# Kernel tuning notes

Hardware: AMD Instinct MI355X
Metric: run time of the kernel (lower is better)

The kernel has to match this reference:

```python
import jax, jax.numpy as jnp
import numpy as np

TEMPERATURE = 0.07


def setup_inputs() -> dict:
    key = jax.random.key(0)
    k1, k2 = jax.random.split(key)
    features = jax.random.normal(k1, (8192, 512), dtype=jnp.float32)
    targets = jax.random.randint(k2, (8192,), 0, 100, dtype=jnp.int64)
    return {"features": features, "targets": targets}


def reference(features, targets):
    n = features.shape[0]
    # L2 normalize along feature dim (F.normalize, dim=1)
    feats = features / jnp.linalg.norm(features, axis=1, keepdims=True)
    # [N, N] similarity matrix
    sim = jnp.matmul(feats, feats.T) / TEMPERATURE
    # positive-pair mask (same label, excluding self)
    mask = (targets[:, None] == targets[None, :]).astype(sim.dtype)
    mask = mask - jnp.eye(n, dtype=sim.dtype)
    # log_prob = sim - log(sum_j exp(sim_ij)) ; denominator includes the diagonal,
    # exactly as in the torch code. logsumexp is the stable single-pass form.
    log_prob = sim - jax.nn.logsumexp(sim, axis=1, keepdims=True)
    mean_log_prob_pos = jnp.sum(mask * log_prob, axis=1) / jnp.sum(mask, axis=1)
    loss = -jnp.mean(mean_log_prob_pos)
    return loss
```

## Files before the change

### kernel.cpp

```cpp
#include <hip/hip_runtime.h>

#define TEMP 0.07f
#define NSLOT 41

typedef __attribute__((ext_vector_type(4))) float f32x4;
typedef __attribute__((ext_vector_type(4))) int   i32x4;
typedef __attribute__((ext_vector_type(8))) int   i32x8;

__global__ __launch_bounds__(256) void knorm(const float* __restrict__ X,
                                             unsigned char* __restrict__ Fq, int D) {
  int row = blockIdx.x * 4 + (threadIdx.x >> 6);
  int lane = threadIdx.x & 63;
  const float4* xr = (const float4*)(X + (size_t)row * D);
  float4 a = xr[lane];
  float4 b = xr[lane + 64];
  float ss = a.x*a.x + a.y*a.y + a.z*a.z + a.w*a.w
           + b.x*b.x + b.y*b.y + b.z*b.z + b.w*b.w;
  #pragma unroll
  for (int off = 1; off < 64; off <<= 1) ss += __shfl_xor(ss, off, 64);
  float r = rsqrtf(ss);
  int lo = 0, hi = 0;
  lo = __builtin_amdgcn_cvt_pk_fp8_f32(a.x*r, a.y*r, lo, false);
  lo = __builtin_amdgcn_cvt_pk_fp8_f32(a.z*r, a.w*r, lo, true);
  hi = __builtin_amdgcn_cvt_pk_fp8_f32(b.x*r, b.y*r, hi, false);
  hi = __builtin_amdgcn_cvt_pk_fp8_f32(b.z*r, b.w*r, hi, true);
  unsigned char* op = Fq + (size_t)row * D;
  *(int*)(op + lane * 4)       = lo;
  *(int*)(op + 256 + lane * 4) = hi;
}

__global__ __launch_bounds__(256, 1)
void kmain(const unsigned char* __restrict__ F, const int* __restrict__ tgt,
           float* __restrict__ psum, float* __restrict__ pmask, int N, int D) {
  __shared__ __align__(16) unsigned char Bs[2][64 * 512];
  __shared__ float cred[2][4][128];
  __shared__ int tgts[512];

  const int tid  = threadIdx.x;
  const int lane = tid & 63;
  const int wave = tid >> 6;
  const int quad = lane >> 4;
  const int l15  = lane & 15;

  const int b = blockIdx.x;
  int I, t0, ntiles;
  if (b < 512) { I = b & 63; t0 = (b >> 6) * 4; ntiles = 4; }
  else         { I = b - 512; t0 = 32;          ntiles = 1; }
  const int rowbase = I * 128;
  int cb[4];
  #pragma unroll
  for (int c = 0; c < 4; ++c) cb[c] = ((I + t0 + c) & 63) << 7;

  i32x8 af[2][4];
  #pragma unroll
  for (int mi = 0; mi < 2; ++mi) {
    const unsigned char* rp = F + (size_t)(rowbase + wave*32 + mi*16 + l15) * 512 + quad*32;
    #pragma unroll
    for (int ks = 0; ks < 4; ++ks) {
      i32x4 lo = *(const i32x4*)(rp + ks*128);
      i32x4 hi = *(const i32x4*)(rp + ks*128 + 16);
      af[mi][ks] = __builtin_shufflevector(lo, hi, 0,1,2,3,4,5,6,7);
    }
  }

  int trow[2][4];
  #pragma unroll
  for (int mi = 0; mi < 2; ++mi)
    #pragma unroll
    for (int r = 0; r < 4; ++r)
      trow[mi][r] = tgt[rowbase + wave*32 + mi*16 + quad*4 + r];

  #pragma unroll
  for (int it = 0; it < 2; ++it) {
    int i = tid + it * 256;
    tgts[i] = tgt[(((I + t0 + (i >> 7)) & 63) << 7) + (i & 127)];
  }

  float se[2][4], ms[2][4];
  #pragma unroll
  for (int mi = 0; mi < 2; ++mi)
    #pragma unroll
    for (int r = 0; r < 4; ++r) { se[mi][r] = 0.f; ms[mi][r] = 0.f; }
  f32x4 ce[4][2], cm[4][2];
  #pragma unroll
  for (int c = 0; c < 4; ++c)
    #pragma unroll
    for (int h = 0; h < 2; ++h) {
      ce[c][h] = (f32x4){0,0,0,0};
      cm[c][h] = (f32x4){0,0,0,0};
    }

  const float C1 = (1.0f / TEMP) * 1.4426950408889634f;
  const float C0 = -C1;
  const int sw0 = (quad * 2) ^ (l15 & 7);

  auto STAGE = [&](int s) {
    const int rbase = cb[s >> 1] + (s & 1) * 64;
    unsigned char* db = &Bs[0][0] + (s & 1) * 32768;
    #pragma unroll
    for (int it = 0; it < 8; ++it) {
      const int L   = it * 256 + tid;
      const int row = L >> 5;
      const int ks  = (L & 31) ^ (row & 7);
      const unsigned char* gp = F + (size_t)(rbase + row) * 512 + ks * 16;
      __builtin_amdgcn_global_load_lds(
          (const __attribute__((address_space(1))) void*)gp,
          (__attribute__((address_space(3))) void*)(db + L * 16), 16, 0, 0);
    }
  };

  auto COMP = [&](int p) {
    const int c = p >> 1, h = p & 1;
    f32x4 acc[2][4];
    #pragma unroll
    for (int mi = 0; mi < 2; ++mi)
      #pragma unroll
      for (int ni = 0; ni < 4; ++ni)
        acc[mi][ni] = (f32x4){0.f, 0.f, 0.f, 0.f};

    const unsigned char* bb  = &Bs[0][0] + (p & 1) * 32768 + l15 * 512;
    const unsigned char* bp0 = bb + sw0 * 16;
    const unsigned char* bp1 = bb + (sw0 ^ 1) * 16;

    #pragma unroll
    for (int ks = 0; ks < 4; ++ks) {
      #pragma unroll
      for (int ni = 0; ni < 4; ++ni) {
        i32x4 b0 = *(const i32x4*)(bp0 + ni*8192 + ks*128);
        i32x4 b1 = *(const i32x4*)(bp1 + ni*8192 + ks*128);
        i32x8 bv = __builtin_shufflevector(b0, b1, 0,1,2,3,4,5,6,7);
        acc[0][ni] = __builtin_amdgcn_mfma_scale_f32_16x16x128_f8f6f4(
            af[0][ks], bv, acc[0][ni], 0, 0, 0, 0x7F7F7F7F, 0, 0x7F7F7F7F);
        acc[1][ni] = __builtin_amdgcn_mfma_scale_f32_16x16x128_f8f6f4(
            af[1][ks], bv, acc[1][ni], 0, 0, 0, 0x7F7F7F7F, 0, 0x7F7F7F7F);
      }
    }

    int tcg[4];
    #pragma unroll
    for (int ni = 0; ni < 4; ++ni) tcg[ni] = tgts[c*128 + h*64 + ni*16 + l15];
    #pragma unroll
    for (int mi = 0; mi < 2; ++mi)
      #pragma unroll
      for (int ni = 0; ni < 4; ++ni)
        #pragma unroll
        for (int r = 0; r < 4; ++r) {
          float v = acc[mi][ni][r];
          float e = __builtin_amdgcn_exp2f(fmaf(v, C1, C0));
          se[mi][r]    += e;
          ce[c][h][ni] += e;
          if (tcg[ni] == trow[mi][r]) { ms[mi][r] += v; cm[c][h][ni] += v; }
        }
  };

  __syncthreads();
  STAGE(0);

  const int lim = 2 * ntiles;
  #pragma unroll
  for (int p = 0; p < 8; ++p) {
    if (p < lim) {
      if (p + 1 < lim) {
        STAGE(p + 1);
        asm volatile("s_waitcnt vmcnt(8)" ::: "memory");
      } else {
        asm volatile("s_waitcnt vmcnt(0)" ::: "memory");
      }
      __builtin_amdgcn_s_barrier();
      COMP(p);
      __builtin_amdgcn_s_barrier();
    }
  }

  const int stc = (b < 512) ? (b >> 6) : 8;
  #pragma unroll
  for (int mi = 0; mi < 2; ++mi)
    #pragma unroll
    for (int r = 0; r < 4; ++r) {
      float s = se[mi][r], m = ms[mi][r];
      #pragma unroll
      for (int off = 1; off < 16; off <<= 1) {
        s += __shfl_xor(s, off, 64);
        m += __shfl_xor(m, off, 64);
      }
      if (l15 == 0) {
        int row = rowbase + wave*32 + mi*16 + quad*4 + r;
        psum [(size_t)stc * N + row] = s;
        pmask[(size_t)stc * N + row] = m;
      }
    }

  #pragma unroll
  for (int c = 0; c < 4; ++c) {
    const bool havec = (c < ntiles) && (t0 + c != 0);
    if (havec) {
      #pragma unroll
      for (int g = 0; g < 2; ++g)
        #pragma unroll
        for (int ni = 0; ni < 4; ++ni) {
          float e = ce[c][g][ni];
          float m = cm[c][g][ni];
          e += __shfl_xor(e, 16, 64); e += __shfl_xor(e, 32, 64);
          m += __shfl_xor(m, 16, 64); m += __shfl_xor(m, 32, 64);
          if (quad == 0) {
            cred[0][wave][g*64 + ni*16 + l15] = e;
            cred[1][wave][g*64 + ni*16 + l15] = m;
          }
        }
    }
    __syncthreads();
    if (havec && tid < 128) {
      float s = cred[0][0][tid] + cred[0][1][tid] + cred[0][2][tid] + cred[0][3][tid];
      float m = cred[1][0][tid] + cred[1][1][tid] + cred[1][2][tid] + cred[1][3][tid];
      const int slot = 8 + t0 + c;
      psum [(size_t)slot * N + cb[c] + tid] = s;
      pmask[(size_t)slot * N + cb[c] + tid] = m;
    }
    __syncthreads();
  }
}

__global__ __launch_bounds__(256) void kfinal(
    const float* __restrict__ psum, const float* __restrict__ pmask,
    const int* __restrict__ tgt, float* __restrict__ out, int N, int nslot) {
  __shared__ int h[128];
  __shared__ float wsum[4];
  const int tid = threadIdx.x;
  if (tid < 128) h[tid] = 0;
  __syncthreads();
  for (int i = tid; i < N; i += 256) atomicAdd(&h[tgt[i] & 127], 1);
  __syncthreads();

  const int i = blockIdx.x * 256 + tid;
  float s = 0.f, m = 0.f;
  #pragma unroll 8
  for (int sp = 0; sp < nslot; ++sp) {
    s += psum[(size_t)sp * N + i];
    m += pmask[(size_t)sp * N + i];
  }
  const float invT = 1.0f / TEMP;
  float cnt = (float)(h[tgt[i] & 127] - 1);
  float term = (m - 1.0f) * invT / cnt - (logf(s) + invT);
  #pragma unroll
  for (int off = 1; off < 64; off <<= 1) term += __shfl_xor(term, off, 64);
  if ((tid & 63) == 0) wsum[tid >> 6] = term;
  __syncthreads();
  if (tid == 0)
    atomicAdd(out, -(wsum[0] + wsum[1] + wsum[2] + wsum[3]) / (float)N);
}

extern "C" void kernel_launch(void* const* d_in, const int* in_sizes, int n_in,
                              void* d_out, int out_size, void* d_ws, size_t ws_size,
                              hipStream_t stream) {
  const float* X  = (const float*)d_in[0];
  const int* tgt  = (const int*)d_in[1];
  float* out      = (float*)d_out;
  const int N = in_sizes[1];
  const int D = in_sizes[0] / N;

  char* w = (char*)d_ws;
  unsigned char* Fq = (unsigned char*)w;
  size_t off = (size_t)N * D;
  float* psum  = (float*)(w + off);
  size_t psz = (size_t)NSLOT * N * sizeof(float);
  off += psz;
  float* pmask = (float*)(w + off);

  hipMemsetAsync(d_out, 0, sizeof(float), stream);
  hipMemsetAsync(psum, 0, 2 * psz, stream);
  knorm<<<N / 4, 256, 0, stream>>>(X, Fq, D);
  kmain<<<512 + 32, 256, 0, stream>>>(Fq, tgt, psum, pmask, N, D);
  kfinal<<<N / 256, 256, 0, stream>>>(psum, pmask, tgt, out, N, NSLOT);
}
```

Measured before the change: 133.6 us.

## Remove memset launches and restructure symmetric tile schedule with in-kernel zeroing

Drops the two hipMemsetAsync calls: the output scalar is now zeroed inside knorm, and the partial-sum slots that would otherwise be unwritten are zeroed by the diagonal block inside kmain. The upper-triangular tile assignment changes from a cyclic wraparound scheme to a paired row-chunk scheme (Q and 15-Q) using 80 slots, so each block covers a contiguous range of column tiles. The intent is to cut launch and memset overhead while keeping the 544 blocks balanced. In exchange, kfinal has to reduce more partial slots.

```diff
diff --git a/kernel.cpp b/kernel.cpp
--- a/kernel.cpp
+++ b/kernel.cpp
@@ -1,14 +1,17 @@
 #include <hip/hip_runtime.h>
 
 #define TEMP 0.07f
-#define NSLOT 41
+#define NROWSLOT 16
+#define NSLOT 80
 
 typedef __attribute__((ext_vector_type(4))) float f32x4;
 typedef __attribute__((ext_vector_type(4))) int   i32x4;
 typedef __attribute__((ext_vector_type(8))) int   i32x8;
 
 __global__ __launch_bounds__(256) void knorm(const float* __restrict__ X,
-                                             unsigned char* __restrict__ Fq, int D) {
+                                             unsigned char* __restrict__ Fq,
+                                             float* __restrict__ out, int D) {
+  if (blockIdx.x == 0 && threadIdx.x == 0) *out = 0.f;
   int row = blockIdx.x * 4 + (threadIdx.x >> 6);
   int lane = threadIdx.x & 63;
   const float4* xr = (const float4*)(X + (size_t)row * D);
@@ -42,14 +45,29 @@
   const int quad = lane >> 4;
   const int l15  = lane & 15;
 
-  const int b = blockIdx.x;
-  int I, t0, ntiles;
-  if (b < 512) { I = b & 63; t0 = (b >> 6) * 4; ntiles = 4; }
-  else         { I = b - 512; t0 = 32;          ntiles = 1; }
+  const int b  = blockIdx.x;
+  const int Q  = b & 7;
+  const int k  = b >> 3;
+  const int M1 = 15 - Q;
+  int mc, I;
+  if (k < 4*Q + 1) { mc = Q;  I = k; }
+  else if (k < 62) { mc = M1; I = k - 4*Q - 1; }
+  else if (k < 65) { mc = Q;  I = 4*Q + 1 + (k - 62); }
+  else             { mc = M1; I = 4*M1 + 1 + (k - 65); }
+  const int jlo     = (4*mc > I) ? 4*mc : I;
+  const int ntiles  = 4*mc + 4 - jlo;
+  const int lim     = 2 * ntiles;
   const int rowbase = I * 128;
-  int cb[4];
-  #pragma unroll
-  for (int c = 0; c < 4; ++c) cb[c] = ((I + t0 + c) & 63) << 7;
+  const bool diagblk = (jlo == I);
+
+  if (diagblk) {
+    float* P = (tid >> 7) ? pmask : psum;
+    const int r = tid & 127;
+    for (int mp = 0; mp < mc; ++mp)
+      P[(size_t)mp * N + rowbase + r] = 0.f;
+    for (int s = I; s < 64; ++s)
+      P[(size_t)(NROWSLOT + s) * N + rowbase + r] = 0.f;
+  }
 
   i32x8 af[2][4];
   #pragma unroll
@@ -70,11 +88,8 @@
     for (int r = 0; r < 4; ++r)
       trow[mi][r] = tgt[rowbase + wave*32 + mi*16 + quad*4 + r];
 
-  #pragma unroll
-  for (int it = 0; it < 2; ++it) {
-    int i = tid + it * 256;
-    tgts[i] = tgt[(((I + t0 + (i >> 7)) & 63) << 7) + (i & 127)];
-  }
+  for (int i = tid; i < ntiles * 128; i += 256)
+    tgts[i] = tgt[jlo * 128 + i];
 
   float se[2][4], ms[2][4];
   #pragma unroll
@@ -95,7 +110,7 @@
   const int sw0 = (quad * 2) ^ (l15 & 7);
 
   auto STAGE = [&](int s) {
-    const int rbase = cb[s >> 1] + (s & 1) * 64;
+    const int rbase = (jlo + (s >> 1)) * 128 + (s & 1) * 64;
     unsigned char* db = &Bs[0][0] + (s & 1) * 32768;
     #pragma unroll
     for (int it = 0; it < 8; ++it) {
@@ -156,7 +171,6 @@
   __syncthreads();
   STAGE(0);
 
-  const int lim = 2 * ntiles;
   #pragma unroll
   for (int p = 0; p < 8; ++p) {
     if (p < lim) {
@@ -172,49 +186,47 @@
     }
   }
 
-  const int stc = (b < 512) ? (b >> 6) : 8;
   #pragma unroll
   for (int mi = 0; mi < 2; ++mi)
     #pragma unroll
     for (int r = 0; r < 4; ++r) {
-      float s = se[mi][r], m = ms[mi][r];
+      float s = se[mi][r], mm = ms[mi][r];
       #pragma unroll
       for (int off = 1; off < 16; off <<= 1) {
-        s += __shfl_xor(s, off, 64);
-        m += __shfl_xor(m, off, 64);
+        s  += __shfl_xor(s, off, 64);
+        mm += __shfl_xor(mm, off, 64);
       }
       if (l15 == 0) {
         int row = rowbase + wave*32 + mi*16 + quad*4 + r;
-        psum [(size_t)stc * N + row] = s;
-        pmask[(size_t)stc * N + row] = m;
+        psum [(size_t)mc * N + row] = s;
+        pmask[(size_t)mc * N + row] = mm;
       }
     }
 
   #pragma unroll
   for (int c = 0; c < 4; ++c) {
-    const bool havec = (c < ntiles) && (t0 + c != 0);
+    const bool havec = (c < ntiles) && !(diagblk && c == 0);
     if (havec) {
       #pragma unroll
       for (int g = 0; g < 2; ++g)
         #pragma unroll
         for (int ni = 0; ni < 4; ++ni) {
-          float e = ce[c][g][ni];
-          float m = cm[c][g][ni];
-          e += __shfl_xor(e, 16, 64); e += __shfl_xor(e, 32, 64);
-          m += __shfl_xor(m, 16, 64); m += __shfl_xor(m, 32, 64);
+          float e  = ce[c][g][ni];
+          float mm = cm[c][g][ni];
+          e  += __shfl_xor(e, 16, 64);  e  += __shfl_xor(e, 32, 64);
+          mm += __shfl_xor(mm, 16, 64); mm += __shfl_xor(mm, 32, 64);
           if (quad == 0) {
             cred[0][wave][g*64 + ni*16 + l15] = e;
-            cred[1][wave][g*64 + ni*16 + l15] = m;
+            cred[1][wave][g*64 + ni*16 + l15] = mm;
           }
         }
     }
     __syncthreads();
     if (havec && tid < 128) {
-      float s = cred[0][0][tid] + cred[0][1][tid] + cred[0][2][tid] + cred[0][3][tid];
-      float m = cred[1][0][tid] + cred[1][1][tid] + cred[1][2][tid] + cred[1][3][tid];
-      const int slot = 8 + t0 + c;
-      psum [(size_t)slot * N + cb[c] + tid] = s;
-      pmask[(size_t)slot * N + cb[c] + tid] = m;
+      float s  = cred[0][0][tid] + cred[0][1][tid] + cred[0][2][tid] + cred[0][3][tid];
+      float mm = cred[1][0][tid] + cred[1][1][tid] + cred[1][2][tid] + cred[1][3][tid];
+      psum [(size_t)(NROWSLOT + I) * N + (jlo + c) * 128 + tid] = s;
+      pmask[(size_t)(NROWSLOT + I) * N + (jlo + c) * 128 + tid] = mm;
     }
     __syncthreads();
   }
@@ -266,9 +278,7 @@
   off += psz;
   float* pmask = (float*)(w + off);
 
-  hipMemsetAsync(d_out, 0, sizeof(float), stream);
-  hipMemsetAsync(psum, 0, 2 * psz, stream);
-  knorm<<<N / 4, 256, 0, stream>>>(X, Fq, D);
-  kmain<<<512 + 32, 256, 0, stream>>>(Fq, tgt, psum, pmask, N, D);
+  knorm<<<N / 4, 256, 0, stream>>>(X, Fq, out, D);
+  kmain<<<544, 256, 0, stream>>>(Fq, tgt, psum, pmask, N, D);
   kfinal<<<N / 256, 256, 0, stream>>>(psum, pmask, tgt, out, N, NSLOT);
 }
```

Measured after the change: 137.2 us. +2.8%, slower.

## Restructure symmetric tile schedule into 256 blocks with triple-buffered staging

Applied to the files above, without the earlier changes.

Reworks the symmetric similarity tiling so each of 256 blocks handles 8 off-diagonal tiles plus its own tile, with the diagonal contribution handled analytically (s starts at 1, m drops the self term). Block staging moves to a 3-deep LDS ring so two tiles are in flight. Column partial sums are written out progressively inside the loop, overlapping that work with compute. The separate output memsets are removed and the output is zeroed inside knorm. This removes the 32-block tail wave and the memset launches, at the cost of more LDS per block and a riskier pipeline and reduction ordering.

```diff
diff --git a/kernel.cpp b/kernel.cpp
--- a/kernel.cpp
+++ b/kernel.cpp
@@ -1,14 +1,16 @@
 #include <hip/hip_runtime.h>
 
 #define TEMP 0.07f
-#define NSLOT 41
+#define NSLOT 35
 
 typedef __attribute__((ext_vector_type(4))) float f32x4;
 typedef __attribute__((ext_vector_type(4))) int   i32x4;
 typedef __attribute__((ext_vector_type(8))) int   i32x8;
 
 __global__ __launch_bounds__(256) void knorm(const float* __restrict__ X,
-                                             unsigned char* __restrict__ Fq, int D) {
+                                             unsigned char* __restrict__ Fq,
+                                             float* __restrict__ out, int D) {
+  if (blockIdx.x == 0 && threadIdx.x == 0) *out = 0.f;
   int row = blockIdx.x * 4 + (threadIdx.x >> 6);
   int lane = threadIdx.x & 63;
   const float4* xr = (const float4*)(X + (size_t)row * D);
@@ -32,9 +34,9 @@
 __global__ __launch_bounds__(256, 1)
 void kmain(const unsigned char* __restrict__ F, const int* __restrict__ tgt,
            float* __restrict__ psum, float* __restrict__ pmask, int N, int D) {
-  __shared__ __align__(16) unsigned char Bs[2][64 * 512];
+  __shared__ __align__(16) unsigned char Bs[3][64 * 512];
   __shared__ float cred[2][4][128];
-  __shared__ int tgts[512];
+  __shared__ int tgts[1024];
 
   const int tid  = threadIdx.x;
   const int lane = tid & 63;
@@ -42,14 +44,10 @@
   const int quad = lane >> 4;
   const int l15  = lane & 15;
 
-  const int b = blockIdx.x;
-  int I, t0, ntiles;
-  if (b < 512) { I = b & 63; t0 = (b >> 6) * 4; ntiles = 4; }
-  else         { I = b - 512; t0 = 32;          ntiles = 1; }
+  const int I  = blockIdx.x & 63;
+  const int q  = blockIdx.x >> 6;
+  const int t0 = q * 8;
   const int rowbase = I * 128;
-  int cb[4];
-  #pragma unroll
-  for (int c = 0; c < 4; ++c) cb[c] = ((I + t0 + c) & 63) << 7;
 
   i32x8 af[2][4];
   #pragma unroll
@@ -71,9 +69,10 @@
       trow[mi][r] = tgt[rowbase + wave*32 + mi*16 + quad*4 + r];
 
   #pragma unroll
-  for (int it = 0; it < 2; ++it) {
+  for (int it = 0; it < 4; ++it) {
     int i = tid + it * 256;
-    tgts[i] = tgt[(((I + t0 + (i >> 7)) & 63) << 7) + (i & 127)];
+    int tile = (I + t0 + 1 + (i >> 7)) & 63;
+    tgts[i] = tgt[tile * 128 + (i & 127)];
   }
 
   float se[2][4], ms[2][4];
@@ -81,22 +80,16 @@
   for (int mi = 0; mi < 2; ++mi)
     #pragma unroll
     for (int r = 0; r < 4; ++r) { se[mi][r] = 0.f; ms[mi][r] = 0.f; }
-  f32x4 ce[4][2], cm[4][2];
-  #pragma unroll
-  for (int c = 0; c < 4; ++c)
-    #pragma unroll
-    for (int h = 0; h < 2; ++h) {
-      ce[c][h] = (f32x4){0,0,0,0};
-      cm[c][h] = (f32x4){0,0,0,0};
-    }
+  f32x4 ce[2], cm[2];
 
   const float C1 = (1.0f / TEMP) * 1.4426950408889634f;
   const float C0 = -C1;
   const int sw0 = (quad * 2) ^ (l15 & 7);
 
   auto STAGE = [&](int s) {
-    const int rbase = cb[s >> 1] + (s & 1) * 64;
-    unsigned char* db = &Bs[0][0] + (s & 1) * 32768;
+    const int tile  = (I + t0 + 1 + (s >> 1)) & 63;
+    const int rbase = tile * 128 + (s & 1) * 64;
+    unsigned char* db = &Bs[0][0] + (s % 3) * 32768;
     #pragma unroll
     for (int it = 0; it < 8; ++it) {
       const int L   = it * 256 + tid;
@@ -109,8 +102,35 @@
     }
   };
 
-  auto COMP = [&](int p) {
+  __syncthreads();
+  STAGE(0);
+  STAGE(1);
+
+  #pragma unroll
+  for (int p = 0; p < 16; ++p) {
+    if (p < 15) asm volatile("s_waitcnt vmcnt(8)" ::: "memory");
+    else        asm volatile("s_waitcnt vmcnt(0)" ::: "memory");
+    __builtin_amdgcn_s_barrier();
+
+    if (p + 2 < 16) STAGE(p + 2);
+
+    if (p >= 2 && (p & 1) == 0) {
+      const int cf = (p - 2) >> 1;
+      const int tf = t0 + 1 + cf;
+      const int Jf = (I + tf) & 63;
+      const int col = tid & 127, arr = tid >> 7;
+      float v = cred[arr][0][col] + cred[arr][1][col]
+              + cred[arr][2][col] + cred[arr][3][col];
+      (arr ? pmask : psum)[(size_t)(3 + tf) * N + Jf * 128 + col] = v;
+    }
+
     const int c = p >> 1, h = p & 1;
+    const bool lc = !(q == 3 && c == 7);
+    if (h == 0) {
+      ce[0] = (f32x4){0,0,0,0}; ce[1] = (f32x4){0,0,0,0};
+      cm[0] = (f32x4){0,0,0,0}; cm[1] = (f32x4){0,0,0,0};
+    }
+
     f32x4 acc[2][4];
     #pragma unroll
     for (int mi = 0; mi < 2; ++mi)
@@ -118,7 +138,7 @@
       for (int ni = 0; ni < 4; ++ni)
         acc[mi][ni] = (f32x4){0.f, 0.f, 0.f, 0.f};
 
-    const unsigned char* bb  = &Bs[0][0] + (p & 1) * 32768 + l15 * 512;
+    const unsigned char* bb  = &Bs[0][0] + (p % 3) * 32768 + l15 * 512;
     const unsigned char* bp0 = bb + sw0 * 16;
     const unsigned char* bp1 = bb + (sw0 ^ 1) * 16;
 
@@ -147,59 +167,17 @@
         for (int r = 0; r < 4; ++r) {
           float v = acc[mi][ni][r];
           float e = __builtin_amdgcn_exp2f(fmaf(v, C1, C0));
-          se[mi][r]    += e;
-          ce[c][h][ni] += e;
-          if (tcg[ni] == trow[mi][r]) { ms[mi][r] += v; cm[c][h][ni] += v; }
+          bool mt = (tcg[ni] == trow[mi][r]);
+          se[mi][r] += e; if (mt) ms[mi][r] += v;
+          if (lc) { ce[h][ni] += e; if (mt) cm[h][ni] += v; }
         }
-  };
-
-  __syncthreads();
-  STAGE(0);
-
-  const int lim = 2 * ntiles;
-  #pragma unroll
-  for (int p = 0; p < 8; ++p) {
-    if (p < lim) {
-      if (p + 1 < lim) {
-        STAGE(p + 1);
-        asm volatile("s_waitcnt vmcnt(8)" ::: "memory");
-      } else {
-        asm volatile("s_waitcnt vmcnt(0)" ::: "memory");
-      }
-      __builtin_amdgcn_s_barrier();
-      COMP(p);
-      __builtin_amdgcn_s_barrier();
-    }
-  }
-
-  const int stc = (b < 512) ? (b >> 6) : 8;
-  #pragma unroll
-  for (int mi = 0; mi < 2; ++mi)
-    #pragma unroll
-    for (int r = 0; r < 4; ++r) {
-      float s = se[mi][r], m = ms[mi][r];
-      #pragma unroll
-      for (int off = 1; off < 16; off <<= 1) {
-        s += __shfl_xor(s, off, 64);
-        m += __shfl_xor(m, off, 64);
-      }
-      if (l15 == 0) {
-        int row = rowbase + wave*32 + mi*16 + quad*4 + r;
-        psum [(size_t)stc * N + row] = s;
-        pmask[(size_t)stc * N + row] = m;
-      }
-    }
-
-  #pragma unroll
-  for (int c = 0; c < 4; ++c) {
-    const bool havec = (c < ntiles) && (t0 + c != 0);
-    if (havec) {
+
+    if (h == 1 && lc) {
       #pragma unroll
       for (int g = 0; g < 2; ++g)
         #pragma unroll
         for (int ni = 0; ni < 4; ++ni) {
-          float e = ce[c][g][ni];
-          float m = cm[c][g][ni];
+          float e = ce[g][ni], m = cm[g][ni];
           e += __shfl_xor(e, 16, 64); e += __shfl_xor(e, 32, 64);
           m += __shfl_xor(m, 16, 64); m += __shfl_xor(m, 32, 64);
           if (quad == 0) {
@@ -207,17 +185,36 @@
             cred[1][wave][g*64 + ni*16 + l15] = m;
           }
         }
-    }
-    __syncthreads();
-    if (havec && tid < 128) {
-      float s = cred[0][0][tid] + cred[0][1][tid] + cred[0][2][tid] + cred[0][3][tid];
-      float m = cred[1][0][tid] + cred[1][1][tid] + cred[1][2][tid] + cred[1][3][tid];
-      const int slot = 8 + t0 + c;
-      psum [(size_t)slot * N + cb[c] + tid] = s;
-      pmask[(size_t)slot * N + cb[c] + tid] = m;
-    }
-    __syncthreads();
-  }
+      asm volatile("s_waitcnt lgkmcnt(0)" ::: "memory");
+    }
+  }
+
+  if (q != 3) {
+    __builtin_amdgcn_s_barrier();
+    const int tf = t0 + 8;
+    const int Jf = (I + tf) & 63;
+    const int col = tid & 127, arr = tid >> 7;
+    float v = cred[arr][0][col] + cred[arr][1][col]
+            + cred[arr][2][col] + cred[arr][3][col];
+    (arr ? pmask : psum)[(size_t)(3 + tf) * N + Jf * 128 + col] = v;
+  }
+
+  #pragma unroll
+  for (int mi = 0; mi < 2; ++mi)
+    #pragma unroll
+    for (int r = 0; r < 4; ++r) {
+      float sv = se[mi][r], mv = ms[mi][r];
+      #pragma unroll
+      for (int off = 1; off < 16; off <<= 1) {
+        sv += __shfl_xor(sv, off, 64);
+        mv += __shfl_xor(mv, off, 64);
+      }
+      if (l15 == 0) {
+        int row = rowbase + wave*32 + mi*16 + quad*4 + r;
+        psum [(size_t)q * N + row] = sv;
+        pmask[(size_t)q * N + row] = mv;
+      }
+    }
 }
 
 __global__ __launch_bounds__(256) void kfinal(
@@ -232,15 +229,15 @@
   __syncthreads();
 
   const int i = blockIdx.x * 256 + tid;
-  float s = 0.f, m = 0.f;
-  #pragma unroll 8
+  float s = 1.f, m = 0.f;
+  #pragma unroll 7
   for (int sp = 0; sp < nslot; ++sp) {
     s += psum[(size_t)sp * N + i];
     m += pmask[(size_t)sp * N + i];
   }
   const float invT = 1.0f / TEMP;
   float cnt = (float)(h[tgt[i] & 127] - 1);
-  float term = (m - 1.0f) * invT / cnt - (logf(s) + invT);
+  float term = m * invT / cnt - (logf(s) + invT);
   #pragma unroll
   for (int off = 1; off < 64; off <<= 1) term += __shfl_xor(term, off, 64);
   if ((tid & 63) == 0) wsum[tid >> 6] = term;
@@ -266,9 +263,7 @@
   off += psz;
   float* pmask = (float*)(w + off);
 
-  hipMemsetAsync(d_out, 0, sizeof(float), stream);
-  hipMemsetAsync(psum, 0, 2 * psz, stream);
-  knorm<<<N / 4, 256, 0, stream>>>(X, Fq, D);
-  kmain<<<512 + 32, 256, 0, stream>>>(Fq, tgt, psum, pmask, N, D);
+  knorm<<<N / 4, 256, 0, stream>>>(X, Fq, out, D);
+  kmain<<<256, 256, 0, stream>>>(Fq, tgt, psum, pmask, N, D);
   kfinal<<<N / 256, 256, 0, stream>>>(psum, pmask, tgt, out, N, NSLOT);
 }
```

Result: slower. 241.5 us (+80.8%).
